# Kernel optimization log

Measured on AMD Instinct MI355X. Metric: run time of the kernel, lower is better.

## Reference

```python
import jax, jax.numpy as jnp
import numpy as np

N = 100000   # nodes
E = 640000   # edges (before self-loops)
G = 1000     # graphs in batch
D_IN = 100
D = 128
EPS = 1e-5


def setup_inputs() -> dict:
    key = jax.random.key(0)
    ks = jax.random.split(key, 12)
    x = jax.random.normal(ks[0], (N, D_IN), dtype=jnp.float32)
    edge_index = jax.random.randint(ks[1], (2, E), 0, N, dtype=jnp.int64)
    edge_weight = jax.random.uniform(ks[2], (E,), dtype=jnp.float32)
    batch = jnp.sort(jax.random.randint(ks[3], (N,), 0, G, dtype=jnp.int64))
    def glorot(k, shape):
        fan = shape[0]
        return jax.random.normal(k, shape, dtype=jnp.float32) / np.float32(np.sqrt(fan))
    return {
        "x": x, "edge_index": edge_index, "edge_weight": edge_weight, "batch": batch,
        "W0": glorot(ks[4], (D_IN, D)), "b0": jnp.zeros((D,), jnp.float32),
        "W1": glorot(ks[5], (D, D)),    "b1": jnp.zeros((D,), jnp.float32),
        "W2": glorot(ks[6], (D, D)),    "b2": jnp.zeros((D,), jnp.float32),
        "gamma": jnp.ones((3, D), jnp.float32), "beta": jnp.zeros((3, D), jnp.float32),
        "run_mean": jnp.zeros((3, D), jnp.float32), "run_var": jnp.ones((3, D), jnp.float32),
        "Wout": glorot(ks[7], (D, 1)), "bout": jnp.zeros((1,), jnp.float32),
    }


def reference(x, edge_index, edge_weight, batch, W0, b0, W1, b1, W2, b2,
              gamma, beta, run_mean, run_var, Wout, bout):
    n = x.shape[0]
    # add self-loops with weight 1 (GCNConv default)
    loop = jnp.arange(n, dtype=edge_index.dtype)
    src = jnp.concatenate([edge_index[0], loop])
    dst = jnp.concatenate([edge_index[1], loop])
    ew = jnp.concatenate([edge_weight, jnp.ones((n,), edge_weight.dtype)])
    # symmetric normalization: D^{-1/2} A D^{-1/2}
    deg = jax.ops.segment_sum(ew, dst, num_segments=n)
    dinv = jnp.where(deg > 0, jax.lax.rsqrt(deg), 0.0)
    norm = dinv[src] * ew * dinv[dst]            # [E+N]

    def gcn_bn_relu(h, W, b, g, bt, rm, rv):
        h = h @ W                                 # linear first (cheaper gather dim)
        agg = jax.ops.segment_sum(h[src] * norm[:, None], dst, num_segments=n)
        agg = agg + b
        # BatchNorm1d in eval mode (running stats); dropout is identity in eval
        agg = g * (agg - rm) * jax.lax.rsqrt(rv + EPS) + bt
        return jax.nn.relu(agg)

    h = gcn_bn_relu(x, W0, b0, gamma[0], beta[0], run_mean[0], run_var[0])
    h = gcn_bn_relu(h, W1, b1, gamma[1], beta[1], run_mean[1], run_var[1])
    h = gcn_bn_relu(h, W2, b2, gamma[2], beta[2], run_mean[2], run_var[2])

    # global mean pool over graphs
    counts = jax.ops.segment_sum(jnp.ones((n,), h.dtype), batch, num_segments=G)
    pooled = jax.ops.segment_sum(h, batch, num_segments=G) / jnp.maximum(counts, 1.0)[:, None]
    return pooled @ Wout + bout
```

## Files before the change

### kernel.cpp

```cpp
#include <hip/hip_runtime.h>

#define BN_EPS 1e-5f
#define BINCAP 32

static inline size_t align_up(size_t x, size_t a) { return (x + a - 1) & ~(a - 1); }

typedef __attribute__((ext_vector_type(8))) short bf16x8;
typedef __attribute__((ext_vector_type(4))) float f32x4;

__device__ __forceinline__ void bf16split(float v, unsigned short& hi, unsigned short& lo) {
    unsigned u = __float_as_uint(v);
    unsigned rh = (u + 0x7FFFu + ((u >> 16) & 1u)) >> 16;
    float fh = __uint_as_float(rh << 16);
    hi = (unsigned short)rh;
    float rem = v - fh;
    unsigned u2 = __float_as_uint(rem);
    lo = (unsigned short)((u2 + 0x7FFFu + ((u2 >> 16) & 1u)) >> 16);
}

__device__ __forceinline__ unsigned short bf16rne(float v) {
    unsigned u = __float_as_uint(v);
    return (unsigned short)((u + 0x7FFFu + ((u >> 16) & 1u)) >> 16);
}

__device__ __forceinline__ float chlo(unsigned u) { return __uint_as_float(u << 16); }
__device__ __forceinline__ float chhi(unsigned u) { return __uint_as_float(u & 0xffff0000u); }



__global__ void place_prep_kernel(const int* __restrict__ src, const int* __restrict__ dst,
                                  const float* __restrict__ ew,
                                  int* __restrict__ cntc, int2* __restrict__ bins, int E,
                                  const float* __restrict__ W0, const float* __restrict__ W1,
                                  const float* __restrict__ W2, int K0,
                                  unsigned short* __restrict__ Whi, unsigned short* __restrict__ Wlo,
                                  const float* __restrict__ gamma, const float* __restrict__ beta,
                                  const float* __restrict__ rm, const float* __restrict__ rv,
                                  const float* __restrict__ b0, const float* __restrict__ b1,
                                  const float* __restrict__ b2,
                                  float* __restrict__ scale, float* __restrict__ shiftv,
                                  const int* __restrict__ batch, int* __restrict__ gstart,
                                  int N, int G) {
    int tid = blockIdx.x * blockDim.x + threadIdx.x;
    int nth = gridDim.x * blockDim.x;

    int nquads = (E + 3) >> 2;
    for (int q = tid; q < nquads; q += nth) {
        int e0 = q * 4;
        if (e0 + 4 <= E) {
            int4   s4 = *(const int4*)(src + e0);
            int4   d4 = *(const int4*)(dst + e0);
            float4 w4 = *(const float4*)(ew + e0);
            int p0 = atomicAdd(&cntc[d4.x], 1);
            int p1 = atomicAdd(&cntc[d4.y], 1);
            int p2 = atomicAdd(&cntc[d4.z], 1);
            int p3 = atomicAdd(&cntc[d4.w], 1);
            if (p0 < BINCAP) bins[(size_t)d4.x * BINCAP + p0] = make_int2(s4.x, __float_as_int(w4.x));
            if (p1 < BINCAP) bins[(size_t)d4.y * BINCAP + p1] = make_int2(s4.y, __float_as_int(w4.y));
            if (p2 < BINCAP) bins[(size_t)d4.z * BINCAP + p2] = make_int2(s4.z, __float_as_int(w4.z));
            if (p3 < BINCAP) bins[(size_t)d4.w * BINCAP + p3] = make_int2(s4.w, __float_as_int(w4.w));
        } else {
            for (int e = e0; e < E; ++e) {
                int d = dst[e];
                int pos = atomicAdd(&cntc[d], 1);
                if (pos < BINCAP)
                    bins[(size_t)d * BINCAP + pos] = make_int2(src[e], __float_as_int(ew[e]));
            }
        }
    }

    int total = 3 * 32 * 64 * 8 + 384 + N;
    for (int idx = tid; idx < total; idx += nth) {
        if (idx < 3 * 32 * 64 * 8) {
            int j    = idx & 7;
            int lane = (idx >> 3) & 63;
            int f    = (idx >> 9) & 31;
            int l    = idx >> 14;
            int ct = f >> 2, k0c = f & 3;
            int quad = lane >> 4, m16 = lane & 15;
            int n = ct * 16 + m16;
            int k = k0c * 32 + quad * 8 + j;
            const float* W = (l == 0) ? W0 : (l == 1) ? W1 : W2;
            int Kl = (l == 0) ? K0 : 128;
            float v = (k < Kl) ? W[(size_t)k * 128 + n] : 0.f;
            unsigned short hi, lo;
            bf16split(v, hi, lo);
            Whi[idx] = hi;
            Wlo[idx] = lo;
        } else if (idx < 3 * 32 * 64 * 8 + 384) {
            int t = idx - 3 * 32 * 64 * 8;
            int l = t >> 7, j = t & 127;
            const float* bs = (l == 0) ? b0 : (l == 1) ? b1 : b2;
            float sc = gamma[t] * rsqrtf(rv[t] + BN_EPS);
            scale[t] = sc;
            shiftv[t] = beta[t] + (bs[j] - rm[t]) * sc;
        } else {
            int i = idx - (3 * 32 * 64 * 8 + 384);
            int b = batch[i];
            int prev = (i == 0) ? -1 : batch[i - 1];
            for (int g = prev + 1; g <= b; ++g) gstart[g] = i;
            if (i == N - 1) {
                for (int g = b + 1; g <= G; ++g) gstart[g] = N;
            }
        }
    }
}


__device__ __forceinline__ void mfma_tail(const bf16x8 ah[4], const bf16x8 al[4],
                                          const unsigned short* __restrict__ Whi,
                                          const unsigned short* __restrict__ Wlo,
                                          unsigned short* __restrict__ Yh,
                                          const float* __restrict__ dinv,
                                          int row0, int quad, int m16, int lane, int N) {
    const bf16x8* Wh8 = (const bf16x8*)Whi;
    const bf16x8* Wl8 = (const bf16x8*)Wlo;

    f32x4 acc[8];
    #pragma unroll
    for (int ct = 0; ct < 8; ++ct) acc[ct] = (f32x4){0.f, 0.f, 0.f, 0.f};

    bf16x8 bh[2][4], bl[2][4];
    #pragma unroll
    for (int k0c = 0; k0c < 4; ++k0c) {
        bh[0][k0c] = Wh8[k0c * 64 + lane];
        bl[0][k0c] = Wl8[k0c * 64 + lane];
    }

    __builtin_amdgcn_s_setprio(1);
    #pragma unroll
    for (int ct = 0; ct < 8; ++ct) {
        int cur = ct & 1, nxt = cur ^ 1;
        if (ct < 7) {
            #pragma unroll
            for (int k0c = 0; k0c < 4; ++k0c) {
                bh[nxt][k0c] = Wh8[((ct + 1) * 4 + k0c) * 64 + lane];
                bl[nxt][k0c] = Wl8[((ct + 1) * 4 + k0c) * 64 + lane];
            }
        }
        #pragma unroll
        for (int k0c = 0; k0c < 4; ++k0c) {
            acc[ct] = __builtin_amdgcn_mfma_f32_16x16x32_bf16(ah[k0c], bh[cur][k0c], acc[ct], 0, 0, 0);
            acc[ct] = __builtin_amdgcn_mfma_f32_16x16x32_bf16(ah[k0c], bl[cur][k0c], acc[ct], 0, 0, 0);
            acc[ct] = __builtin_amdgcn_mfma_f32_16x16x32_bf16(al[k0c], bh[cur][k0c], acc[ct], 0, 0, 0);
        }
    }
    __builtin_amdgcn_s_setprio(0);

    #pragma unroll
    for (int rg = 0; rg < 4; ++rg) {
        int row = row0 + quad * 4 + rg;
        if (row < N) {
            float dr = dinv[row];
            #pragma unroll
            for (int ct = 0; ct < 8; ++ct)
                Yh[(size_t)row * 128 + ct * 16 + m16] = bf16rne(acc[ct][rg] * dr);
        }
    }
}


__launch_bounds__(256, 2)
__global__ void deginv_gemm0_kernel(const int* __restrict__ cntc, const int2* __restrict__ bins,
                                    float* __restrict__ dinv,
                                    const float* __restrict__ x, int D_IN,
                                    const unsigned short* __restrict__ Whi,
                                    const unsigned short* __restrict__ Wlo,
                                    unsigned short* __restrict__ Yh, int N) {
    int tid = threadIdx.x;
    int tile = blockIdx.x;

    {
        int node = tile * 64 + (tid & 63);
        if (node < N) {
            int cnt = cntc[node]; if (cnt > BINCAP) cnt = BINCAP;
            const int2* b = bins + (size_t)node * BINCAP;
            float s = 0.f;
            for (int j = 0; j < cnt; ++j) s += __int_as_float(b[j].y);
            dinv[node] = rsqrtf(s + 1.0f);
        }
    }
    __syncthreads();

    int wid = tid >> 6, lane = tid & 63;
    int quad = lane >> 4, m16 = lane & 15;
    int row0 = tile * 64 + wid * 16;

    int arow = row0 + m16;
    if (arow > N - 1) arow = N - 1;
    const float* xr = x + (size_t)arow * D_IN;

    bf16x8 ah[4], al[4];
    #pragma unroll
    for (int k0c = 0; k0c < 4; ++k0c) {
        int kb = k0c * 32 + quad * 8;
        float vs[8];
        if (kb + 8 <= D_IN) {
            float4 v0 = *((const float4*)(xr + kb));
            float4 v1 = *((const float4*)(xr + kb + 4));
            vs[0] = v0.x; vs[1] = v0.y; vs[2] = v0.z; vs[3] = v0.w;
            vs[4] = v1.x; vs[5] = v1.y; vs[6] = v1.z; vs[7] = v1.w;
        } else {
            #pragma unroll
            for (int j = 0; j < 8; ++j) vs[j] = (kb + j < D_IN) ? xr[kb + j] : 0.f;
        }
        #pragma unroll
        for (int j = 0; j < 8; ++j) {
            unsigned short hi, lo;
            bf16split(vs[j], hi, lo);
            ah[k0c][j] = (short)hi;
            al[k0c][j] = (short)lo;
        }
    }

    mfma_tail(ah, al, Whi, Wlo, Yh, dinv, row0, quad, m16, lane, N);
}


__device__ __forceinline__ void gather_pair(const unsigned* __restrict__ Yh32,
                                            int2 pr0, int m0, int2 pr1, int m1,
                                            int lane,
                                            float& ax0, float& ay0, float& ax1, float& ay1) {
    int mr0 = (m0 + 7) & ~7, mr1 = (m1 + 7) & ~7;
    int mr = mr0 > mr1 ? mr0 : mr1;
    for (int j = 0; j < mr; j += 8) {
        int a0 = __builtin_amdgcn_readlane(pr0.x, j);
        int a1 = __builtin_amdgcn_readlane(pr0.x, j + 1);
        int a2 = __builtin_amdgcn_readlane(pr0.x, j + 2);
        int a3 = __builtin_amdgcn_readlane(pr0.x, j + 3);
        int a4 = __builtin_amdgcn_readlane(pr0.x, j + 4);
        int a5 = __builtin_amdgcn_readlane(pr0.x, j + 5);
        int a6 = __builtin_amdgcn_readlane(pr0.x, j + 6);
        int a7 = __builtin_amdgcn_readlane(pr0.x, j + 7);
        int b0 = __builtin_amdgcn_readlane(pr1.x, j);
        int b1 = __builtin_amdgcn_readlane(pr1.x, j + 1);
        int b2 = __builtin_amdgcn_readlane(pr1.x, j + 2);
        int b3 = __builtin_amdgcn_readlane(pr1.x, j + 3);
        int b4 = __builtin_amdgcn_readlane(pr1.x, j + 4);
        int b5 = __builtin_amdgcn_readlane(pr1.x, j + 5);
        int b6 = __builtin_amdgcn_readlane(pr1.x, j + 6);
        int b7 = __builtin_amdgcn_readlane(pr1.x, j + 7);
        float wa0 = __int_as_float(__builtin_amdgcn_readlane(pr0.y, j));
        float wa1 = __int_as_float(__builtin_amdgcn_readlane(pr0.y, j + 1));
        float wa2 = __int_as_float(__builtin_amdgcn_readlane(pr0.y, j + 2));
        float wa3 = __int_as_float(__builtin_amdgcn_readlane(pr0.y, j + 3));
        float wa4 = __int_as_float(__builtin_amdgcn_readlane(pr0.y, j + 4));
        float wa5 = __int_as_float(__builtin_amdgcn_readlane(pr0.y, j + 5));
        float wa6 = __int_as_float(__builtin_amdgcn_readlane(pr0.y, j + 6));
        float wa7 = __int_as_float(__builtin_amdgcn_readlane(pr0.y, j + 7));
        float wb0 = __int_as_float(__builtin_amdgcn_readlane(pr1.y, j));
        float wb1 = __int_as_float(__builtin_amdgcn_readlane(pr1.y, j + 1));
        float wb2 = __int_as_float(__builtin_amdgcn_readlane(pr1.y, j + 2));
        float wb3 = __int_as_float(__builtin_amdgcn_readlane(pr1.y, j + 3));
        float wb4 = __int_as_float(__builtin_amdgcn_readlane(pr1.y, j + 4));
        float wb5 = __int_as_float(__builtin_amdgcn_readlane(pr1.y, j + 5));
        float wb6 = __int_as_float(__builtin_amdgcn_readlane(pr1.y, j + 6));
        float wb7 = __int_as_float(__builtin_amdgcn_readlane(pr1.y, j + 7));
        unsigned ua0 = Yh32[(size_t)a0 * 64 + lane];
        unsigned ua1 = Yh32[(size_t)a1 * 64 + lane];
        unsigned ua2 = Yh32[(size_t)a2 * 64 + lane];
        unsigned ua3 = Yh32[(size_t)a3 * 64 + lane];
        unsigned ua4 = Yh32[(size_t)a4 * 64 + lane];
        unsigned ua5 = Yh32[(size_t)a5 * 64 + lane];
        unsigned ua6 = Yh32[(size_t)a6 * 64 + lane];
        unsigned ua7 = Yh32[(size_t)a7 * 64 + lane];
        unsigned ub0 = Yh32[(size_t)b0 * 64 + lane];
        unsigned ub1 = Yh32[(size_t)b1 * 64 + lane];
        unsigned ub2 = Yh32[(size_t)b2 * 64 + lane];
        unsigned ub3 = Yh32[(size_t)b3 * 64 + lane];
        unsigned ub4 = Yh32[(size_t)b4 * 64 + lane];
        unsigned ub5 = Yh32[(size_t)b5 * 64 + lane];
        unsigned ub6 = Yh32[(size_t)b6 * 64 + lane];
        unsigned ub7 = Yh32[(size_t)b7 * 64 + lane];
        ax0 += chlo(ua0) * wa0; ay0 += chhi(ua0) * wa0;
        ax0 += chlo(ua1) * wa1; ay0 += chhi(ua1) * wa1;
        ax0 += chlo(ua2) * wa2; ay0 += chhi(ua2) * wa2;
        ax0 += chlo(ua3) * wa3; ay0 += chhi(ua3) * wa3;
        ax0 += chlo(ua4) * wa4; ay0 += chhi(ua4) * wa4;
        ax0 += chlo(ua5) * wa5; ay0 += chhi(ua5) * wa5;
        ax0 += chlo(ua6) * wa6; ay0 += chhi(ua6) * wa6;
        ax0 += chlo(ua7) * wa7; ay0 += chhi(ua7) * wa7;
        ax1 += chlo(ub0) * wb0; ay1 += chhi(ub0) * wb0;
        ax1 += chlo(ub1) * wb1; ay1 += chhi(ub1) * wb1;
        ax1 += chlo(ub2) * wb2; ay1 += chhi(ub2) * wb2;
        ax1 += chlo(ub3) * wb3; ay1 += chhi(ub3) * wb3;
        ax1 += chlo(ub4) * wb4; ay1 += chhi(ub4) * wb4;
        ax1 += chlo(ub5) * wb5; ay1 += chhi(ub5) * wb5;
        ax1 += chlo(ub6) * wb6; ay1 += chhi(ub6) * wb6;
        ax1 += chlo(ub7) * wb7; ay1 += chhi(ub7) * wb7;
    }
}


__launch_bounds__(64, 4)
__global__ void fused_agg_gemm_kernel(
        const unsigned* __restrict__ Yh_in,
        const int2* __restrict__ bins, const int* __restrict__ cntc,
        const float* __restrict__ dinv,
        const float* __restrict__ scale, const float* __restrict__ shift,
        const unsigned short* __restrict__ Whi, const unsigned short* __restrict__ Wlo,
        unsigned short* __restrict__ Yh_out, int N) {
    __shared__ float sA[16 * 132];
    int lane = threadIdx.x;
    int quad = lane >> 4, m16 = lane & 15;
    int row0 = blockIdx.x * 16;

    float2 sc = ((const float2*)scale)[lane];
    float2 sh = ((const float2*)shift)[lane];

    int mm[16]; float dv[16]; unsigned uh[16]; int2 gg[16];
    #pragma unroll
    for (int i = 0; i < 16; ++i) {
        int n = row0 + i; if (n > N - 1) n = N - 1;
        mm[i] = cntc[n];
        dv[i] = dinv[n];
        uh[i] = Yh_in[(size_t)n * 64 + lane];
    }
    #pragma unroll
    for (int i = 0; i < 16; ++i) {
        int n = row0 + i; if (n > N - 1) n = N - 1;
        int m = mm[i]; if (m > BINCAP) m = BINCAP;
        mm[i] = m;
        gg[i] = (lane < m) ? bins[(size_t)n * BINCAP + lane] : make_int2(n, 0);
    }

    #pragma unroll
    for (int i = 0; i < 16; i += 2) {
        float ax0 = chlo(uh[i]),     ay0 = chhi(uh[i]);
        float ax1 = chlo(uh[i + 1]), ay1 = chhi(uh[i + 1]);
        gather_pair(Yh_in, gg[i], mm[i], gg[i + 1], mm[i + 1], lane, ax0, ay0, ax1, ay1);
        float dv0 = dv[i], dv1 = dv[i + 1];
        float ox0 = fmaxf(ax0 * dv0 * sc.x + sh.x, 0.f);
        float oy0 = fmaxf(ay0 * dv0 * sc.y + sh.y, 0.f);
        float ox1 = fmaxf(ax1 * dv1 * sc.x + sh.x, 0.f);
        float oy1 = fmaxf(ay1 * dv1 * sc.y + sh.y, 0.f);
        *((float2*)&sA[i * 132 + 2 * lane])       = make_float2(ox0, oy0);
        *((float2*)&sA[(i + 1) * 132 + 2 * lane]) = make_float2(ox1, oy1);
    }

    asm volatile("s_waitcnt lgkmcnt(0)" ::: "memory");
    __builtin_amdgcn_sched_barrier(0);

    bf16x8 ah[4], al[4];
    #pragma unroll
    for (int k0c = 0; k0c < 4; ++k0c) {
        float4 v0 = *((const float4*)&sA[m16 * 132 + k0c * 32 + quad * 8]);
        float4 v1 = *((const float4*)&sA[m16 * 132 + k0c * 32 + quad * 8 + 4]);
        float vs[8] = {v0.x, v0.y, v0.z, v0.w, v1.x, v1.y, v1.z, v1.w};
        #pragma unroll
        for (int j = 0; j < 8; ++j) {
            unsigned short hi, lo;
            bf16split(vs[j], hi, lo);
            ah[k0c][j] = (short)hi;
            al[k0c][j] = (short)lo;
        }
    }

    mfma_tail(ah, al, Whi, Wlo, Yh_out, dinv, row0, quad, m16, lane, N);
}


__launch_bounds__(64)
__global__ void agg3_kernel(const unsigned* __restrict__ Yh32,
                            const int2* __restrict__ bins, const int* __restrict__ cntc,
                            const float* __restrict__ dinv,
                            const float* __restrict__ scale, const float* __restrict__ shift,
                            const float* __restrict__ Wout,
                            float* __restrict__ snode, int N) {
    int pairid = blockIdx.x;
    int lane = threadIdx.x;
    int n0 = pairid * 2;
    if (n0 >= N) return;
    int n1 = n0 + 1; if (n1 > N - 1) n1 = n0;

    int m0 = cntc[n0];
    int m1 = cntc[n1];
    float d0 = dinv[n0], d1 = dinv[n1];
    unsigned uh0 = Yh32[(size_t)n0 * 64 + lane];
    unsigned uh1 = Yh32[(size_t)n1 * 64 + lane];
    if (m0 > BINCAP) m0 = BINCAP;
    if (m1 > BINCAP) m1 = BINCAP;
    int2 pr0 = (lane < m0) ? bins[(size_t)n0 * BINCAP + lane] : make_int2(n0, 0);
    int2 pr1 = (lane < m1) ? bins[(size_t)n1 * BINCAP + lane] : make_int2(n1, 0);

    float ax0 = chlo(uh0), ay0 = chhi(uh0);
    float ax1 = chlo(uh1), ay1 = chhi(uh1);
    gather_pair(Yh32, pr0, m0, pr1, m1, lane, ax0, ay0, ax1, ay1);

    float2 sc = ((const float2*)scale)[lane];
    float2 sh = ((const float2*)shift)[lane];
    float2 w  = ((const float2*)Wout)[lane];
    float ox0 = fmaxf(ax0 * d0 * sc.x + sh.x, 0.f);
    float oy0 = fmaxf(ay0 * d0 * sc.y + sh.y, 0.f);
    float ox1 = fmaxf(ax1 * d1 * sc.x + sh.x, 0.f);
    float oy1 = fmaxf(ay1 * d1 * sc.y + sh.y, 0.f);
    float s0 = ox0 * w.x + oy0 * w.y;
    float s1 = ox1 * w.x + oy1 * w.y;
    #pragma unroll
    for (int off = 32; off > 0; off >>= 1) {
        s0 += __shfl_down(s0, off, 64);
        s1 += __shfl_down(s1, off, 64);
    }
    if (lane == 0) {
        snode[n0] = s0;
        if (n1 != n0) snode[n1] = s1;
    }
}


__launch_bounds__(256)
__global__ void pool3_kernel(const float* __restrict__ snode, const int* __restrict__ gstart,
                             const float* __restrict__ bout, float* __restrict__ out, int G) {
    int g = blockIdx.x;
    int beg = gstart[g], end = gstart[g + 1];
    int t = threadIdx.x;
    float acc = 0.f;
    for (int n = beg + t; n < end; n += 256) acc += snode[n];
    __shared__ float lds[256];
    lds[t] = acc;
    __syncthreads();
    if (t < 64) lds[t] = lds[t] + lds[t + 64] + lds[t + 128] + lds[t + 192];
    __syncthreads();
    if (t < 64) {
        float s = lds[t];
        #pragma unroll
        for (int off = 32; off > 0; off >>= 1) s += __shfl_down(s, off, 64);
        if (t == 0) {
            float cntf = (float)(end - beg);
            out[g] = s / fmaxf(cntf, 1.0f) + bout[0];
        }
    }
}


extern "C" void kernel_launch(void* const* d_in, const int* in_sizes, int n_in,
                              void* d_out, int out_size, void* d_ws, size_t ws_size,
                              hipStream_t stream) {
    const float* x     = (const float*)d_in[0];
    const int*   ei    = (const int*)d_in[1];
    const float* ew    = (const float*)d_in[2];
    const int*   batch = (const int*)d_in[3];
    const float* W0 = (const float*)d_in[4];
    const float* b0 = (const float*)d_in[5];
    const float* W1 = (const float*)d_in[6];
    const float* b1 = (const float*)d_in[7];
    const float* W2 = (const float*)d_in[8];
    const float* b2 = (const float*)d_in[9];
    const float* gamma = (const float*)d_in[10];
    const float* beta  = (const float*)d_in[11];
    const float* rmean = (const float*)d_in[12];
    const float* rvar  = (const float*)d_in[13];
    const float* Wout  = (const float*)d_in[14];
    const float* bout  = (const float*)d_in[15];

    const int E = in_sizes[2];
    const int N = in_sizes[3];
    const int D_IN = in_sizes[0] / N;
    const int G = out_size;

    const int* src = ei;
    const int* dst = ei + E;

    char* ws = (char*)d_ws;
    size_t off = 0;
    float* dinv  = (float*)(ws + off); off = align_up(off + (size_t)N * 4, 256);
    int* cntc    = (int*)(ws + off);   off = align_up(off + (size_t)N * 4, 256);
    int* gstart  = (int*)(ws + off);   off = align_up(off + ((size_t)G + 1) * 4, 256);
    int2* bins   = (int2*)(ws + off);  off = align_up(off + (size_t)N * BINCAP * 8, 256);
    unsigned short* YAh = (unsigned short*)(ws + off); off = align_up(off + (size_t)N * 128 * 2, 256);
    unsigned short* YBh = (unsigned short*)(ws + off); off = align_up(off + (size_t)N * 128 * 2, 256);
    unsigned short* Whi = (unsigned short*)(ws + off); off = align_up(off + 3 * 16384 * 2, 256);
    unsigned short* Wlo = (unsigned short*)(ws + off); off = align_up(off + 3 * 16384 * 2, 256);
    float* scale = (float*)(ws + off); off = align_up(off + 3 * 128 * 4, 256);
    float* shift = (float*)(ws + off); off = align_up(off + 3 * 128 * 4, 256);
    float* snode = (float*)(ws + off); off = align_up(off + (size_t)N * 4, 256);
    (void)ws_size;

    hipMemsetAsync(cntc, 0, (size_t)N * 4, stream);

    const int tB = 256;

    {
        int nquads = (E + 3) / 4;
        int total  = 3 * 32 * 64 * 8 + 384 + N;
        int work = nquads > total ? nquads : total;
        place_prep_kernel<<<(work + tB - 1) / tB, tB, 0, stream>>>(
            src, dst, ew, cntc, bins, E,
            W0, W1, W2, D_IN, Whi, Wlo,
            gamma, beta, rmean, rvar, b0, b1, b2, scale, shift,
            batch, gstart, N, G);
    }

    deginv_gemm0_kernel<<<(N + 63) / 64, 256, 0, stream>>>(
        cntc, bins, dinv, x, D_IN, Whi, Wlo, YAh, N);

    int fused_blocks = (N + 15) / 16;

    fused_agg_gemm_kernel<<<fused_blocks, 64, 0, stream>>>(
        (const unsigned*)YAh, bins, cntc, dinv,
        scale, shift, Whi + 16384, Wlo + 16384, YBh, N);
    fused_agg_gemm_kernel<<<fused_blocks, 64, 0, stream>>>(
        (const unsigned*)YBh, bins, cntc, dinv,
        scale + 128, shift + 128, Whi + 2 * 16384, Wlo + 2 * 16384, YAh, N);
    agg3_kernel<<<(N + 1) / 2, 64, 0, stream>>>((const unsigned*)YAh,
        bins, cntc, dinv, scale + 256, shift + 256, Wout, snode, N);

    pool3_kernel<<<G, 256, 0, stream>>>(snode, gstart, bout, (float*)d_out, G);
}
```

Baseline: 302.0 us.

## Fold symmetric normalization into edge weights instead of scaling GEMM outputs

Adds a normfix kernel that rewrites each binned edge weight to ew*dinv[src]*dinv[dst] once after degrees are known. The GEMM epilogue no longer multiplies rows by dinv, and the aggregation kernels scale the self-loop term by dinv^2 and drop the post-aggregation dinv multiply. This moves the normalization arithmetic out of three layers into one pass over edges, but adds an extra kernel launch and a read-modify-write over the bin array. It also reorders the epilogue store loop to iterate by column tile first.

```diff
diff --git a/kernel.cpp b/kernel.cpp
--- a/kernel.cpp
+++ b/kernel.cpp
@@ -107,11 +107,25 @@
 }
 
 
+__global__ void normfix_kernel(const int* __restrict__ cntc, int2* __restrict__ bins,
+                               const float* __restrict__ dinv, int N) {
+    int i = blockIdx.x * blockDim.x + threadIdx.x;
+    if (i >= N) return;
+    int cnt = cntc[i]; if (cnt > BINCAP) cnt = BINCAP;
+    float di = dinv[i];
+    int2* b = bins + (size_t)i * BINCAP;
+    for (int j = 0; j < cnt; ++j) {
+        int2 pr = b[j];
+        float w = __int_as_float(pr.y) * dinv[pr.x] * di;
+        b[j].y = __float_as_int(w);
+    }
+}
+
+
 __device__ __forceinline__ void mfma_tail(const bf16x8 ah[4], const bf16x8 al[4],
                                           const unsigned short* __restrict__ Whi,
                                           const unsigned short* __restrict__ Wlo,
                                           unsigned short* __restrict__ Yh,
-                                          const float* __restrict__ dinv,
                                           int row0, int quad, int m16, int lane, int N) {
     const bf16x8* Wh8 = (const bf16x8*)Whi;
     const bf16x8* Wl8 = (const bf16x8*)Wlo;
@@ -148,13 +162,12 @@
     __builtin_amdgcn_s_setprio(0);
 
     #pragma unroll
-    for (int rg = 0; rg < 4; ++rg) {
-        int row = row0 + quad * 4 + rg;
-        if (row < N) {
-            float dr = dinv[row];
-            #pragma unroll
-            for (int ct = 0; ct < 8; ++ct)
-                Yh[(size_t)row * 128 + ct * 16 + m16] = bf16rne(acc[ct][rg] * dr);
+    for (int ct = 0; ct < 8; ++ct) {
+        #pragma unroll
+        for (int rg = 0; rg < 4; ++rg) {
+            int row = row0 + quad * 4 + rg;
+            if (row < N)
+                Yh[(size_t)row * 128 + ct * 16 + m16] = bf16rne(acc[ct][rg]);
         }
     }
 }
@@ -213,7 +226,7 @@
         }
     }
 
-    mfma_tail(ah, al, Whi, Wlo, Yh, dinv, row0, quad, m16, lane, N);
+    mfma_tail(ah, al, Whi, Wlo, Yh, row0, quad, m16, lane, N);
 }
 
 
@@ -326,14 +339,14 @@
 
     #pragma unroll
     for (int i = 0; i < 16; i += 2) {
-        float ax0 = chlo(uh[i]),     ay0 = chhi(uh[i]);
-        float ax1 = chlo(uh[i + 1]), ay1 = chhi(uh[i + 1]);
+        float w00 = dv[i] * dv[i], w01 = dv[i + 1] * dv[i + 1];
+        float ax0 = chlo(uh[i]) * w00,     ay0 = chhi(uh[i]) * w00;
+        float ax1 = chlo(uh[i + 1]) * w01, ay1 = chhi(uh[i + 1]) * w01;
         gather_pair(Yh_in, gg[i], mm[i], gg[i + 1], mm[i + 1], lane, ax0, ay0, ax1, ay1);
-        float dv0 = dv[i], dv1 = dv[i + 1];
-        float ox0 = fmaxf(ax0 * dv0 * sc.x + sh.x, 0.f);
-        float oy0 = fmaxf(ay0 * dv0 * sc.y + sh.y, 0.f);
-        float ox1 = fmaxf(ax1 * dv1 * sc.x + sh.x, 0.f);
-        float oy1 = fmaxf(ay1 * dv1 * sc.y + sh.y, 0.f);
+        float ox0 = fmaxf(ax0 * sc.x + sh.x, 0.f);
+        float oy0 = fmaxf(ay0 * sc.y + sh.y, 0.f);
+        float ox1 = fmaxf(ax1 * sc.x + sh.x, 0.f);
+        float oy1 = fmaxf(ay1 * sc.y + sh.y, 0.f);
         *((float2*)&sA[i * 132 + 2 * lane])       = make_float2(ox0, oy0);
         *((float2*)&sA[(i + 1) * 132 + 2 * lane]) = make_float2(ox1, oy1);
     }
@@ -356,7 +369,7 @@
         }
     }
 
-    mfma_tail(ah, al, Whi, Wlo, Yh_out, dinv, row0, quad, m16, lane, N);
+    mfma_tail(ah, al, Whi, Wlo, Yh_out, row0, quad, m16, lane, N);
 }
 
 
@@ -383,17 +396,18 @@
     int2 pr0 = (lane < m0) ? bins[(size_t)n0 * BINCAP + lane] : make_int2(n0, 0);
     int2 pr1 = (lane < m1) ? bins[(size_t)n1 * BINCAP + lane] : make_int2(n1, 0);
 
-    float ax0 = chlo(uh0), ay0 = chhi(uh0);
-    float ax1 = chlo(uh1), ay1 = chhi(uh1);
+    float w00 = d0 * d0, w01 = d1 * d1;
+    float ax0 = chlo(uh0) * w00, ay0 = chhi(uh0) * w00;
+    float ax1 = chlo(uh1) * w01, ay1 = chhi(uh1) * w01;
     gather_pair(Yh32, pr0, m0, pr1, m1, lane, ax0, ay0, ax1, ay1);
 
     float2 sc = ((const float2*)scale)[lane];
     float2 sh = ((const float2*)shift)[lane];
     float2 w  = ((const float2*)Wout)[lane];
-    float ox0 = fmaxf(ax0 * d0 * sc.x + sh.x, 0.f);
-    float oy0 = fmaxf(ay0 * d0 * sc.y + sh.y, 0.f);
-    float ox1 = fmaxf(ax1 * d1 * sc.x + sh.x, 0.f);
-    float oy1 = fmaxf(ay1 * d1 * sc.y + sh.y, 0.f);
+    float ox0 = fmaxf(ax0 * sc.x + sh.x, 0.f);
+    float oy0 = fmaxf(ay0 * sc.y + sh.y, 0.f);
+    float ox1 = fmaxf(ax1 * sc.x + sh.x, 0.f);
+    float oy1 = fmaxf(ay1 * sc.y + sh.y, 0.f);
     float s0 = ox0 * w.x + oy0 * w.y;
     float s1 = ox1 * w.x + oy1 * w.y;
     #pragma unroll
@@ -494,6 +508,8 @@
     deginv_gemm0_kernel<<<(N + 63) / 64, 256, 0, stream>>>(
         cntc, bins, dinv, x, D_IN, Whi, Wlo, YAh, N);
 
+    normfix_kernel<<<(N + tB - 1) / tB, tB, 0, stream>>>(cntc, bins, dinv, N);
+
     int fused_blocks = (N + 15) / 16;
 
     fused_agg_gemm_kernel<<<fused_blocks, 64, 0, stream>>>(
```

Result: slower. 313.4 us (+3.8%).
